# Performance work log

Measured on AMD Instinct MI355X. Metric: run time of the kernel, lower is better.

Reference implementation:

```python
import jax, jax.numpy as jnp
import numpy as np
import math

M = 8                      # multiplicity (channels per irrep)
COMBOS = [(0,0,0),(0,1,1),(1,0,1),(1,1,0),(1,1,1),(2,1,1)]  # (edge_l, node_l, out_l)

def _cg_coeff(j1, m1, j2, m2, j3, m3):
    # standard (Racah) complex Clebsch-Gordan coefficient <j1 m1 j2 m2 | j3 m3>
    if m3 != m1 + m2:
        return 0.0
    f = math.factorial
    vmin = max(0, j2 - j3 - m1, j1 + m2 - j3)
    vmax = min(j1 + j2 - j3, j1 - m1, j2 + m2)
    pref = (2*j3 + 1) * f(j3+j1-j2) * f(j3-j1+j2) * f(j1+j2-j3) / f(j1+j2+j3+1)
    pref *= f(j3+m3) * f(j3-m3) * f(j1-m1) * f(j1+m1) * f(j2-m2) * f(j2+m2)
    s = 0.0
    for v in range(vmin, vmax + 1):
        s += (-1)**v / (f(v) * f(j1+j2-j3-v) * f(j1-m1-v) * f(j2+m2-v)
                        * f(j3-j2+m1+v) * f(j3-j1-m2+v))
    return math.sqrt(pref) * s

def _su2_cg(l1, l2, l3):
    C = np.zeros((2*l1+1, 2*l2+1, 2*l3+1), dtype=np.complex128)
    for m1 in range(-l1, l1+1):
        for m2 in range(-l2, l2+1):
            m3 = m1 + m2
            if -l3 <= m3 <= l3:
                C[m1+l1, m2+l2, m3+l3] = _cg_coeff(l1, m1, l2, m2, l3, m3)
    return C

def _qmat(l):
    # real -> complex spherical-harmonic change of basis (e3nn convention)
    q = np.zeros((2*l+1, 2*l+1), dtype=np.complex128)
    for m in range(-l, 0):
        q[l+m, l+abs(m)] = 1/np.sqrt(2)
        q[l+m, l-abs(m)] = -1j/np.sqrt(2)
    q[l, l] = 1.0
    for m in range(1, l+1):
        q[l+m, l+abs(m)] = (-1)**m / np.sqrt(2)
        q[l+m, l-abs(m)] = 1j * (-1)**m / np.sqrt(2)
    return (-1j)**l * q

def _so3_cg(l1, l2, l3):
    # real-basis CG, normalized to unit Frobenius norm (matches e3nn _so3_clebsch_gordan)
    C = np.einsum('ij,kl,mn,ikn->jlm', _qmat(l1), _qmat(l2),
                  np.conj(_qmat(l3)).T, _su2_cg(l1, l2, l3))
    assert np.abs(C.imag).max() < 1e-6
    C = C.real
    return C / np.linalg.norm(C)

CG = {c: jnp.asarray(_so3_cg(*c), dtype=jnp.float32) for c in COMBOS}


def setup_inputs() -> dict:
    N, E = 100000, 1600000
    ks = jax.random.split(jax.random.key(0), 6)
    return {
        'node_irreps': jax.random.normal(ks[0], (N, 4*M), jnp.float32),
        'edge_index': jax.random.randint(ks[1], (2, E), 0, N, dtype=jnp.int32),
        'sh0': jax.random.normal(ks[2], (E, 1), jnp.float32),
        'sh1': jax.random.normal(ks[3], (E, 3), jnp.float32),
        'sh2': jax.random.normal(ks[4], (E, 5), jnp.float32),
        'W': jax.random.normal(ks[5], (len(COMBOS), M, M), jnp.float32),
    }


def reference(node_irreps, edge_index, sh0, sh1, sh2, W):
    N, E = node_irreps.shape[0], edge_index.shape[1]
    src = node_irreps[edge_index[0]]                    # gather: [E, 4M]
    feats = {0: src[:, :M][:, :, None],                 # scalar channels [E, M, 1]
             1: src[:, M:].reshape(E, M, 3)}            # vector channels [E, M, 3]
    sh = {0: sh0, 1: sh1, 2: sh2}
    msg = {0: jnp.zeros((E, M, 1), node_irreps.dtype),
           1: jnp.zeros((E, M, 3), node_irreps.dtype)}
    for idx, (le, ln, lo) in enumerate(COMBOS):
        # per-edge CG tensor product: [de,dn,do] x [E,de] x [E,M,dn] -> [E,M,do]
        base = jnp.einsum('ijk,ei,emj->emk', CG[(le, ln, lo)], sh[le], feats[ln])
        # channel-mixing scalar weights (in_channel -> out_channel)
        msg[lo] = msg[lo] + jnp.einsum('io,eik->eok', W[idx], base)
    tgt = edge_index[1]
    agg0 = jax.ops.segment_sum(msg[0].reshape(E, M), tgt, num_segments=N)     # [N, M]
    agg1 = jax.ops.segment_sum(msg[1].reshape(E, 3*M), tgt, num_segments=N)   # [N, 3M]
    return jnp.concatenate([agg0, agg1], axis=1)
```

## Files before the change

kernel.cpp:

```cpp
#include <hip/hip_runtime.h>

#define THREADS 256

typedef float v4f __attribute__((ext_vector_type(4)));


__global__ __launch_bounds__(THREADS) void k_hist2(const int* __restrict__ tgt,
                                                   int* __restrict__ cnt,
                                                   int* __restrict__ ke, int E) {
    int e = blockIdx.x * THREADS + threadIdx.x;
    if (e < E) ke[e] = atomicAdd(&cnt[tgt[e]], 1);
}

__global__ __launch_bounds__(THREADS) void k_scan_partial(const int* __restrict__ cnt,
                                                          int* __restrict__ bsum, int N) {
    __shared__ int lds[THREADS];
    int base = blockIdx.x * 1024 + threadIdx.x * 4;
    int s = 0;
    #pragma unroll
    for (int k = 0; k < 4; ++k) { int i = base + k; if (i < N) s += cnt[i]; }
    lds[threadIdx.x] = s; __syncthreads();
    for (int off = THREADS / 2; off > 0; off >>= 1) {
        if (threadIdx.x < off) lds[threadIdx.x] += lds[threadIdx.x + off];
        __syncthreads();
    }
    if (threadIdx.x == 0) bsum[blockIdx.x] = lds[0];
}

__global__ __launch_bounds__(1024) void k_scan_bsum(int* __restrict__ bsum, int NB) {
    __shared__ int lds[1024];
    int t = threadIdx.x;
    int v = (t < NB) ? bsum[t] : 0;
    lds[t] = v; __syncthreads();
    for (int off = 1; off < 1024; off <<= 1) {
        int x = (t >= off) ? lds[t - off] : 0;
        __syncthreads();
        lds[t] += x;
        __syncthreads();
    }
    if (t < NB) bsum[t] = lds[t] - v;
}

__global__ __launch_bounds__(THREADS) void k_scan_final(const int* __restrict__ cnt,
                                                        const int* __restrict__ bsum,
                                                        int* __restrict__ rowptr,
                                                        int N, int E) {
    __shared__ int lds[THREADS];
    int base = blockIdx.x * 1024 + threadIdx.x * 4;
    int v[4]; int local = 0;
    #pragma unroll
    for (int k = 0; k < 4; ++k) {
        int i = base + k;
        v[k] = (i < N) ? cnt[i] : 0;
        local += v[k];
    }
    lds[threadIdx.x] = local; __syncthreads();
    for (int off = 1; off < THREADS; off <<= 1) {
        int x = (threadIdx.x >= off) ? lds[threadIdx.x - off] : 0;
        __syncthreads();
        lds[threadIdx.x] += x;
        __syncthreads();
    }
    int p = lds[threadIdx.x] - local + bsum[blockIdx.x];
    #pragma unroll
    for (int k = 0; k < 4; ++k) {
        int i = base + k;
        if (i < N) { rowptr[i] = p; p += v[k]; }
    }
    if (blockIdx.x == 0 && threadIdx.x == 0) rowptr[N] = E;
}


__global__ __launch_bounds__(THREADS) void k_scatter(const int* __restrict__ eidx,
                                                     const int* __restrict__ ke,
                                                     const int* __restrict__ rowptr,
                                                     const float* __restrict__ sh0,
                                                     const float* __restrict__ sh1,
                                                     const float* __restrict__ sh2,
                                                     float* __restrict__ payload,
                                                     int E) {
    int e = blockIdx.x * THREADS + threadIdx.x;
    if (e >= E) return;
    int src = eidx[e];
    int tgt = eidx[E + e];
    int pos = rowptr[tgt] + ke[e];

    float4 p0 = make_float4(sh0[e], sh1[3*e+0], sh1[3*e+1], sh1[3*e+2]);
    float4 p1 = make_float4(sh2[5*e+0], sh2[5*e+1], sh2[5*e+2], sh2[5*e+3]);
    float4 p2 = make_float4(sh2[5*e+4], __int_as_float(src), 0.f, 0.f);
    float4 p3 = make_float4(0.f, 0.f, 0.f, 0.f);

    float4* pr = (float4*)(payload + (size_t)pos * 16);
    pr[0] = p0; pr[1] = p1; pr[2] = p2; pr[3] = p3;
}


#define ACC_STRIDE 15

__global__ __launch_bounds__(THREADS) void k_agg2(const float* __restrict__ node,
                                                  const int*   __restrict__ rowptr,
                                                  const float* __restrict__ payload,
                                                  const float* __restrict__ W,
                                                  float*       __restrict__ out, int N) {
    __shared__ float sW[384];
    __shared__ float sAcc[32 * 8 * ACC_STRIDE];
    for (int t = threadIdx.x; t < 384; t += THREADS) sW[t] = W[t];
    __syncthreads();

    constexpr float IS3  = 0.57735026918962576f;
    constexpr float IS6  = 0.40824829046386302f;
    constexpr float IS10 = 0.31622776601683794f;
    constexpr float IS30 = 0.18257418583505536f;

    const int nodeSlot = threadIdx.x >> 3;
    const int i        = threadIdx.x & 7;
    const int n        = blockIdx.x * 32 + nodeSlot;

    float a[14];
    #pragma unroll
    for (int k = 0; k < 14; ++k) a[k] = 0.f;

    if (n < N) {
        const int jbeg = rowptr[n];
        const int jend = rowptr[n + 1];

        if (jbeg < jend) {
            const v4f* pr = (const v4f*)(payload + (size_t)jbeg * 16);
            v4f c0 = __builtin_nontemporal_load(pr + 0);
            v4f c1 = __builtin_nontemporal_load(pr + 1);
            v4f c2 = __builtin_nontemporal_load(pr + 2);

            for (int j = jbeg; j < jend; ++j) {
                v4f n0, n1, n2;
                if (j + 1 < jend) {
                    const v4f* prn = (const v4f*)(payload + (size_t)(j + 1) * 16);
                    n0 = __builtin_nontemporal_load(prn + 0);
                    n1 = __builtin_nontemporal_load(prn + 1);
                    n2 = __builtin_nontemporal_load(prn + 2);
                }

                const int src = __float_as_int(c2.y);
                const float* nr = node + (size_t)src * 32;
                const float f0 = nr[i];
                const float x  = nr[8 + 3*i + 0];
                const float y  = nr[8 + 3*i + 1];
                const float z  = nr[8 + 3*i + 2];

                const float s  = c0.x, u0 = c0.y, u1 = c0.z, u2 = c0.w;
                const float q0 = c1.x, q1 = c1.y, q2 = c1.z, q3 = c1.w, q4 = c2.x;

                const float Q00 = -q2*IS30 - q4*IS10;
                const float Q01 =  q1*IS10;
                const float Q02 =  q0*IS10;
                const float Q11 =  2.0f*q2*IS30;
                const float Q12 =  q3*IS10;
                const float Q22 = -q2*IS30 + q4*IS10;

                a[0]  += s * f0;
                a[1]  += u0*x + u1*y + u2*z;
                a[2]  += s * x;
                a[3]  += s * y;
                a[4]  += s * z;
                a[5]  += f0 * u0;
                a[6]  += f0 * u1;
                a[7]  += f0 * u2;
                a[8]  += u1*z - u2*y;
                a[9]  += u2*x - u0*z;
                a[10] += u0*y - u1*x;
                a[11] += Q00*x + Q01*y + Q02*z;
                a[12] += Q01*x + Q11*y + Q12*z;
                a[13] += Q02*x + Q12*y + Q22*z;

                c0 = n0; c1 = n1; c2 = n2;
            }
        }
    }

    #pragma unroll
    for (int k = 1; k < 8; ++k) a[k] *= IS3;
    #pragma unroll
    for (int k = 8; k < 11; ++k) a[k] *= IS6;

    float* myAcc = &sAcc[(nodeSlot * 8 + i) * ACC_STRIDE];
    #pragma unroll
    for (int k = 0; k < 14; ++k) myAcc[k] = a[k];
    __syncthreads();

    if (n < N) {
        const int o = i;
        float o0 = 0.f, ox = 0.f, oy = 0.f, oz = 0.f;
        #pragma unroll
        for (int ii = 0; ii < 8; ++ii) {
            const float* A = &sAcc[(nodeSlot * 8 + ii) * ACC_STRIDE];
            const float w0 = sW[  0 + ii*8 + o];
            const float w1 = sW[ 64 + ii*8 + o];
            const float w2 = sW[128 + ii*8 + o];
            const float w3 = sW[192 + ii*8 + o];
            const float w4 = sW[256 + ii*8 + o];
            const float w5 = sW[320 + ii*8 + o];
            o0 += w0*A[0]  + w3*A[1];
            ox += w1*A[2]  + w2*A[5] + w4*A[8]  + w5*A[11];
            oy += w1*A[3]  + w2*A[6] + w4*A[9]  + w5*A[12];
            oz += w1*A[4]  + w2*A[7] + w4*A[10] + w5*A[13];
        }
        float* orow = out + (size_t)n * 32;
        orow[o]         = o0;
        orow[8 + 3*o+0] = ox;
        orow[8 + 3*o+1] = oy;
        orow[8 + 3*o+2] = oz;
    }
}


__global__ __launch_bounds__(THREADS) void msg_kernel_atomic(
    const float* __restrict__ node,
    const int*   __restrict__ eidx,
    const float* __restrict__ sh0,
    const float* __restrict__ sh1,
    const float* __restrict__ sh2,
    const float* __restrict__ W,
    float*       __restrict__ out,
    int E)
{
    __shared__ float sW[384];
    for (int t = threadIdx.x; t < 384; t += THREADS) sW[t] = W[t];
    __syncthreads();

    int e = blockIdx.x * THREADS + threadIdx.x;
    if (e >= E) return;

    constexpr float IS3  = 0.57735026918962576f;
    constexpr float IS6  = 0.40824829046386302f;
    constexpr float IS10 = 0.31622776601683794f;
    constexpr float IS30 = 0.18257418583505536f;

    const int src = eidx[e];
    const int tgt = eidx[E + e];

    const float s  = sh0[e];
    const float u0 = sh1[3*e+0], u1 = sh1[3*e+1], u2 = sh1[3*e+2];
    const float q0 = sh2[5*e+0], q1 = sh2[5*e+1], q2 = sh2[5*e+2],
                q3 = sh2[5*e+3], q4 = sh2[5*e+4];

    const float Q00 = -q2*IS30 - q4*IS10;
    const float Q01 =  q1*IS10;
    const float Q02 =  q0*IS10;
    const float Q11 =  2.0f*q2*IS30;
    const float Q12 =  q3*IS10;
    const float Q22 = -q2*IS30 + q4*IS10;

    float f[32];
    {
        const float4* nr = (const float4*)(node + (size_t)src * 32);
        #pragma unroll
        for (int i = 0; i < 8; ++i) {
            float4 v = nr[i];
            f[4*i+0]=v.x; f[4*i+1]=v.y; f[4*i+2]=v.z; f[4*i+3]=v.w;
        }
    }

    float msg[32];
    #pragma unroll
    for (int j = 0; j < 32; ++j) msg[j] = 0.0f;

    const float s13 = s * IS3;

    #pragma unroll
    for (int i = 0; i < 8; ++i) {
        const float f0i = f[i];
        const float x = f[8+3*i+0], y = f[8+3*i+1], z = f[8+3*i+2];
        const float c0  = s * f0i;
        const float c3  = IS3 * (u0*x + u1*y + u2*z);
        const float p2  = IS3 * f0i;
        const float c1x = s13*x, c1y = s13*y, c1z = s13*z;
        const float c2x = p2*u0, c2y = p2*u1, c2z = p2*u2;
        const float c4x = IS6*(u1*z - u2*y);
        const float c4y = IS6*(u2*x - u0*z);
        const float c4z = IS6*(u0*y - u1*x);
        const float c5x = Q00*x + Q01*y + Q02*z;
        const float c5y = Q01*x + Q11*y + Q12*z;
        const float c5z = Q02*x + Q12*y + Q22*z;

        float wr[6][8];
        #pragma unroll
        for (int c = 0; c < 6; ++c) {
            float4 aa = *(const float4*)&sW[c*64 + i*8 + 0];
            float4 bb = *(const float4*)&sW[c*64 + i*8 + 4];
            wr[c][0]=aa.x; wr[c][1]=aa.y; wr[c][2]=aa.z; wr[c][3]=aa.w;
            wr[c][4]=bb.x; wr[c][5]=bb.y; wr[c][6]=bb.z; wr[c][7]=bb.w;
        }

        #pragma unroll
        for (int o = 0; o < 8; ++o) {
            msg[o] += wr[0][o]*c0 + wr[3][o]*c3;
            msg[8+3*o+0] += wr[1][o]*c1x + wr[2][o]*c2x + wr[4][o]*c4x + wr[5][o]*c5x;
            msg[8+3*o+1] += wr[1][o]*c1y + wr[2][o]*c2y + wr[4][o]*c4y + wr[5][o]*c5y;
            msg[8+3*o+2] += wr[1][o]*c1z + wr[2][o]*c2z + wr[4][o]*c4z + wr[5][o]*c5z;
        }
    }

    float* orow = out + (size_t)tgt * 32;
    #pragma unroll
    for (int j = 0; j < 32; ++j) unsafeAtomicAdd(orow + j, msg[j]);
}


extern "C" void kernel_launch(void* const* d_in, const int* in_sizes, int n_in,
                              void* d_out, int out_size, void* d_ws, size_t ws_size,
                              hipStream_t stream) {
    const float* node = (const float*)d_in[0];
    const int*   eidx = (const int*)d_in[1];
    const float* sh0  = (const float*)d_in[2];
    const float* sh1  = (const float*)d_in[3];
    const float* sh2  = (const float*)d_in[4];
    const float* W    = (const float*)d_in[5];
    float* out = (float*)d_out;

    const int E = in_sizes[2];
    const int N = in_sizes[0] / 32;
    const int NB = (N + 1023) / 1024;

    size_t int_words = (size_t)(N + 1) + N + 1024 + (size_t)E;
    size_t pay_off_w = (int_words + 15) & ~(size_t)15;
    size_t need      = (pay_off_w + (size_t)E * 16) * sizeof(float);

    if (ws_size >= need && NB <= 1024) {
        int* rowptr = (int*)d_ws;
        int* cnt    = rowptr + (N + 1);
        int* bsum   = cnt + N;
        int* ke     = bsum + 1024;
        float* payload = (float*)d_ws + pay_off_w;

        hipMemsetAsync(cnt, 0, (size_t)N * sizeof(int), stream);

        k_hist2<<<(E + THREADS - 1) / THREADS, THREADS, 0, stream>>>(eidx + E, cnt, ke, E);
        k_scan_partial<<<NB, THREADS, 0, stream>>>(cnt, bsum, N);
        k_scan_bsum<<<1, 1024, 0, stream>>>(bsum, NB);
        k_scan_final<<<NB, THREADS, 0, stream>>>(cnt, bsum, rowptr, N, E);
        k_scatter<<<(E + THREADS - 1) / THREADS, THREADS, 0, stream>>>(
            eidx, ke, rowptr, sh0, sh1, sh2, payload, E);

        k_agg2<<<(N + 31) / 32, THREADS, 0, stream>>>(node, rowptr, payload, W, out, N);
    } else {
        hipMemsetAsync(d_out, 0, (size_t)out_size * sizeof(float), stream);
        msg_kernel_atomic<<<(E + THREADS - 1) / THREADS, THREADS, 0, stream>>>(
            node, eidx, sh0, sh1, sh2, W, out, E);
    }
}
```

Baseline: 346.6 us.

## Replace per-edge payload scatter with compact edge-index CSR and transposed node layout

Instead of scattering a 64-byte payload per edge (sh values plus src) into CSR order, the scatter now writes only an (edge id, src) pair using an atomic cursor, and the aggregation kernel gathers sh0/sh1/sh2 directly by edge id. Node features are pre-transposed so each lane loads its scalar and vector channel with one 16-byte load, and the per-edge ke array is dropped. This cuts scatter write traffic and workspace, but adds random gathers of sh arrays in the aggregation loop and a second atomic pass.

```diff
diff --git a/kernel.cpp b/kernel.cpp
--- a/kernel.cpp
+++ b/kernel.cpp
@@ -3,13 +3,13 @@
 #define THREADS 256
 
 typedef float v4f __attribute__((ext_vector_type(4)));
-
-
-__global__ __launch_bounds__(THREADS) void k_hist2(const int* __restrict__ tgt,
-                                                   int* __restrict__ cnt,
-                                                   int* __restrict__ ke, int E) {
+typedef int   v2i __attribute__((ext_vector_type(2)));
+
+
+__global__ __launch_bounds__(THREADS) void k_hist(const int* __restrict__ tgt,
+                                                  int* __restrict__ cnt, int E) {
     int e = blockIdx.x * THREADS + threadIdx.x;
-    if (e < E) ke[e] = atomicAdd(&cnt[tgt[e]], 1);
+    if (e < E) atomicAdd(&cnt[tgt[e]], 1);
 }
 
 __global__ __launch_bounds__(THREADS) void k_scan_partial(const int* __restrict__ cnt,
@@ -41,7 +41,7 @@
     if (t < NB) bsum[t] = lds[t] - v;
 }
 
-__global__ __launch_bounds__(THREADS) void k_scan_final(const int* __restrict__ cnt,
+__global__ __launch_bounds__(THREADS) void k_scan_final(int* __restrict__ cnt,
                                                         const int* __restrict__ bsum,
                                                         int* __restrict__ rowptr,
                                                         int N, int E) {
@@ -65,41 +65,48 @@
     #pragma unroll
     for (int k = 0; k < 4; ++k) {
         int i = base + k;
-        if (i < N) { rowptr[i] = p; p += v[k]; }
+        if (i < N) { rowptr[i] = p; cnt[i] = p; p += v[k]; }
     }
     if (blockIdx.x == 0 && threadIdx.x == 0) rowptr[N] = E;
 }
 
 
-__global__ __launch_bounds__(THREADS) void k_scatter(const int* __restrict__ eidx,
-                                                     const int* __restrict__ ke,
-                                                     const int* __restrict__ rowptr,
-                                                     const float* __restrict__ sh0,
-                                                     const float* __restrict__ sh1,
-                                                     const float* __restrict__ sh2,
-                                                     float* __restrict__ payload,
-                                                     int E) {
+__global__ __launch_bounds__(THREADS) void k_ntrans(const float* __restrict__ node,
+                                                    float* __restrict__ nodeT, int NT8) {
+    int t = blockIdx.x * THREADS + threadIdx.x;
+    if (t >= NT8) return;
+    int n = t >> 3, i = t & 7;
+    const float* nr = node + (size_t)n * 32;
+    v4f v;
+    v[0] = nr[i];
+    v[1] = nr[8 + 3*i + 0];
+    v[2] = nr[8 + 3*i + 1];
+    v[3] = nr[8 + 3*i + 2];
+    *(v4f*)(nodeT + (size_t)t * 4) = v;
+}
+
+
+__global__ __launch_bounds__(THREADS) void k_scatter2(const int* __restrict__ eidx,
+                                                      int* __restrict__ cursor,
+                                                      int* __restrict__ col2, int E) {
     int e = blockIdx.x * THREADS + threadIdx.x;
     if (e >= E) return;
     int src = eidx[e];
     int tgt = eidx[E + e];
-    int pos = rowptr[tgt] + ke[e];
-
-    float4 p0 = make_float4(sh0[e], sh1[3*e+0], sh1[3*e+1], sh1[3*e+2]);
-    float4 p1 = make_float4(sh2[5*e+0], sh2[5*e+1], sh2[5*e+2], sh2[5*e+3]);
-    float4 p2 = make_float4(sh2[5*e+4], __int_as_float(src), 0.f, 0.f);
-    float4 p3 = make_float4(0.f, 0.f, 0.f, 0.f);
-
-    float4* pr = (float4*)(payload + (size_t)pos * 16);
-    pr[0] = p0; pr[1] = p1; pr[2] = p2; pr[3] = p3;
+    int pos = atomicAdd(&cursor[tgt], 1);
+    v2i v; v[0] = e; v[1] = src;
+    *(v2i*)(col2 + 2*(size_t)pos) = v;
 }
 
 
 #define ACC_STRIDE 15
 
-__global__ __launch_bounds__(THREADS) void k_agg2(const float* __restrict__ node,
+__global__ __launch_bounds__(THREADS) void k_agg3(const float* __restrict__ nodeT,
                                                   const int*   __restrict__ rowptr,
-                                                  const float* __restrict__ payload,
+                                                  const int*   __restrict__ col2,
+                                                  const float* __restrict__ sh0,
+                                                  const float* __restrict__ sh1,
+                                                  const float* __restrict__ sh2,
                                                   const float* __restrict__ W,
                                                   float*       __restrict__ out, int N) {
     __shared__ float sW[384];
@@ -125,29 +132,35 @@
         const int jend = rowptr[n + 1];
 
         if (jbeg < jend) {
-            const v4f* pr = (const v4f*)(payload + (size_t)jbeg * 16);
-            v4f c0 = __builtin_nontemporal_load(pr + 0);
-            v4f c1 = __builtin_nontemporal_load(pr + 1);
-            v4f c2 = __builtin_nontemporal_load(pr + 2);
+            const int jlast = jend - 1;
+
+            v2i ec = __builtin_nontemporal_load((const v2i*)(col2 + 2*(size_t)jbeg));
+            {
+            }
+            const int e0 = ec[0];
+            float s  = sh0[e0];
+            const float* up = sh1 + 3*(size_t)e0;
+            float u0 = up[0], u1 = up[1], u2 = up[2];
+            const float* qp = sh2 + 5*(size_t)e0;
+            float q0 = qp[0], q1 = qp[1], q2 = qp[2], q3 = qp[3], q4 = qp[4];
+            v4f nf = *(const v4f*)(nodeT + ((size_t)ec[1] * 8 + i) * 4);
+
+            int jn1 = (jbeg + 1 < jend) ? jbeg + 1 : jlast;
+            v2i ecn = __builtin_nontemporal_load((const v2i*)(col2 + 2*(size_t)jn1));
 
             for (int j = jbeg; j < jend; ++j) {
-                v4f n0, n1, n2;
-                if (j + 1 < jend) {
-                    const v4f* prn = (const v4f*)(payload + (size_t)(j + 1) * 16);
-                    n0 = __builtin_nontemporal_load(prn + 0);
-                    n1 = __builtin_nontemporal_load(prn + 1);
-                    n2 = __builtin_nontemporal_load(prn + 2);
-                }
-
-                const int src = __float_as_int(c2.y);
-                const float* nr = node + (size_t)src * 32;
-                const float f0 = nr[i];
-                const float x  = nr[8 + 3*i + 0];
-                const float y  = nr[8 + 3*i + 1];
-                const float z  = nr[8 + 3*i + 2];
-
-                const float s  = c0.x, u0 = c0.y, u1 = c0.z, u2 = c0.w;
-                const float q0 = c1.x, q1 = c1.y, q2 = c1.z, q3 = c1.w, q4 = c2.x;
+                const int en = ecn[0];
+                const float ns = sh0[en];
+                const float* nup = sh1 + 3*(size_t)en;
+                const float nu0 = nup[0], nu1 = nup[1], nu2 = nup[2];
+                const float* nqp = sh2 + 5*(size_t)en;
+                const float nq0 = nqp[0], nq1 = nqp[1], nq2 = nqp[2],
+                            nq3 = nqp[3], nq4 = nqp[4];
+                const v4f nnf = *(const v4f*)(nodeT + ((size_t)ecn[1] * 8 + i) * 4);
+                const int jn2 = (j + 2 < jend) ? j + 2 : jlast;
+                const v2i ec2 = __builtin_nontemporal_load((const v2i*)(col2 + 2*(size_t)jn2));
+
+                const float f0 = nf[0], x = nf[1], y = nf[2], z = nf[3];
 
                 const float Q00 = -q2*IS30 - q4*IS10;
                 const float Q01 =  q1*IS10;
@@ -171,7 +184,9 @@
                 a[12] += Q01*x + Q11*y + Q12*z;
                 a[13] += Q02*x + Q12*y + Q22*z;
 
-                c0 = n0; c1 = n1; c2 = n2;
+                s = ns; u0 = nu0; u1 = nu1; u2 = nu2;
+                q0 = nq0; q1 = nq1; q2 = nq2; q3 = nq3; q4 = nq4;
+                nf = nnf; ecn = ec2;
             }
         }
     }
@@ -320,27 +335,35 @@
     const int N = in_sizes[0] / 32;
     const int NB = (N + 1023) / 1024;
 
-    size_t int_words = (size_t)(N + 1) + N + 1024 + (size_t)E;
-    size_t pay_off_w = (int_words + 15) & ~(size_t)15;
-    size_t need      = (pay_off_w + (size_t)E * 16) * sizeof(float);
+    size_t off = 0;
+    size_t off_rowptr = off; off += (size_t)N + 1;
+    size_t off_cnt    = off; off += (size_t)N;
+    size_t off_bsum   = off; off += 1024;
+    off = (off + 3) & ~(size_t)3;
+    size_t off_col2   = off; off += 2 * (size_t)E;
+    off = (off + 3) & ~(size_t)3;
+    size_t off_nodeT  = off; off += 32 * (size_t)N;
+    size_t need = off * sizeof(float);
 
     if (ws_size >= need && NB <= 1024) {
-        int* rowptr = (int*)d_ws;
-        int* cnt    = rowptr + (N + 1);
-        int* bsum   = cnt + N;
-        int* ke     = bsum + 1024;
-        float* payload = (float*)d_ws + pay_off_w;
+        int* wsI    = (int*)d_ws;
+        int* rowptr = wsI + off_rowptr;
+        int* cnt    = wsI + off_cnt;
+        int* bsum   = wsI + off_bsum;
+        int* col2   = wsI + off_col2;
+        float* nodeT = (float*)d_ws + off_nodeT;
 
         hipMemsetAsync(cnt, 0, (size_t)N * sizeof(int), stream);
 
-        k_hist2<<<(E + THREADS - 1) / THREADS, THREADS, 0, stream>>>(eidx + E, cnt, ke, E);
+        k_hist<<<(E + THREADS - 1) / THREADS, THREADS, 0, stream>>>(eidx + E, cnt, E);
+        k_ntrans<<<(8 * N + THREADS - 1) / THREADS, THREADS, 0, stream>>>(node, nodeT, 8 * N);
         k_scan_partial<<<NB, THREADS, 0, stream>>>(cnt, bsum, N);
         k_scan_bsum<<<1, 1024, 0, stream>>>(bsum, NB);
         k_scan_final<<<NB, THREADS, 0, stream>>>(cnt, bsum, rowptr, N, E);
-        k_scatter<<<(E + THREADS - 1) / THREADS, THREADS, 0, stream>>>(
-            eidx, ke, rowptr, sh0, sh1, sh2, payload, E);
-
-        k_agg2<<<(N + 31) / 32, THREADS, 0, stream>>>(node, rowptr, payload, W, out, N);
+        k_scatter2<<<(E + THREADS - 1) / THREADS, THREADS, 0, stream>>>(eidx, cnt, col2, E);
+
+        k_agg3<<<(N + 31) / 32, THREADS, 0, stream>>>(nodeT, rowptr, col2,
+                                                      sh0, sh1, sh2, W, out, N);
     } else {
         hipMemsetAsync(d_out, 0, (size_t)out_size * sizeof(float), stream);
         msg_kernel_atomic<<<(E + THREADS - 1) / THREADS, THREADS, 0, stream>>>(
```

Result: slower. 468.4 us (+35.1%).

## Write edge payload in edge order with CSR index indirection and deeper prefetch

Applied to the files above, without the earlier changes.

The pack kernel now writes the per-edge spherical-harmonic payload in original edge order with the quadrupole matrix precomputed, so those writes are coalesced rather than scattered. Only a small CSR column array of edge ids is scattered. The aggregation kernel then reads the payload and source ids indirectly through that array and prefetches node features one edge ahead. A fallback path uses an atomic cursor when the workspace is too small to hold the per-edge rank array. The cost is that aggregation reads become random 64-byte gathers plus an extra dependent load chain (col, then esrc, then node).

```diff
diff --git a/kernel.cpp b/kernel.cpp
--- a/kernel.cpp
+++ b/kernel.cpp
@@ -10,6 +10,12 @@
                                                    int* __restrict__ ke, int E) {
     int e = blockIdx.x * THREADS + threadIdx.x;
     if (e < E) ke[e] = atomicAdd(&cnt[tgt[e]], 1);
+}
+
+__global__ __launch_bounds__(THREADS) void k_hist(const int* __restrict__ tgt,
+                                                  int* __restrict__ cnt, int E) {
+    int e = blockIdx.x * THREADS + threadIdx.x;
+    if (e < E) atomicAdd(&cnt[tgt[e]], 1);
 }
 
 __global__ __launch_bounds__(THREADS) void k_scan_partial(const int* __restrict__ cnt,
@@ -41,7 +47,7 @@
     if (t < NB) bsum[t] = lds[t] - v;
 }
 
-__global__ __launch_bounds__(THREADS) void k_scan_final(const int* __restrict__ cnt,
+__global__ __launch_bounds__(THREADS) void k_scan_final(int* __restrict__ cnt,
                                                         const int* __restrict__ bsum,
                                                         int* __restrict__ rowptr,
                                                         int N, int E) {
@@ -65,41 +71,66 @@
     #pragma unroll
     for (int k = 0; k < 4; ++k) {
         int i = base + k;
-        if (i < N) { rowptr[i] = p; p += v[k]; }
+        if (i < N) { rowptr[i] = p; cnt[i] = p; p += v[k]; }
     }
     if (blockIdx.x == 0 && threadIdx.x == 0) rowptr[N] = E;
 }
 
 
-__global__ __launch_bounds__(THREADS) void k_scatter(const int* __restrict__ eidx,
-                                                     const int* __restrict__ ke,
-                                                     const int* __restrict__ rowptr,
-                                                     const float* __restrict__ sh0,
-                                                     const float* __restrict__ sh1,
-                                                     const float* __restrict__ sh2,
-                                                     float* __restrict__ payload,
-                                                     int E) {
+__global__ __launch_bounds__(THREADS) void k_pack(const int* __restrict__ eidx,
+                                                  const int* __restrict__ ke,
+                                                  const int* __restrict__ rowptr,
+                                                  int* __restrict__ cursor,
+                                                  int* __restrict__ col,
+                                                  const float* __restrict__ sh0,
+                                                  const float* __restrict__ sh1,
+                                                  const float* __restrict__ sh2,
+                                                  float* __restrict__ pack,
+                                                  int E) {
     int e = blockIdx.x * THREADS + threadIdx.x;
     if (e >= E) return;
-    int src = eidx[e];
-    int tgt = eidx[E + e];
-    int pos = rowptr[tgt] + ke[e];
-
-    float4 p0 = make_float4(sh0[e], sh1[3*e+0], sh1[3*e+1], sh1[3*e+2]);
-    float4 p1 = make_float4(sh2[5*e+0], sh2[5*e+1], sh2[5*e+2], sh2[5*e+3]);
-    float4 p2 = make_float4(sh2[5*e+4], __int_as_float(src), 0.f, 0.f);
-    float4 p3 = make_float4(0.f, 0.f, 0.f, 0.f);
-
-    float4* pr = (float4*)(payload + (size_t)pos * 16);
-    pr[0] = p0; pr[1] = p1; pr[2] = p2; pr[3] = p3;
+
+    constexpr float IS10 = 0.31622776601683794f;
+    constexpr float IS30 = 0.18257418583505536f;
+
+    const int tgt = eidx[E + e];
+    int pos;
+    if (ke) pos = rowptr[tgt] + ke[e];
+    else    pos = atomicAdd(&cursor[tgt], 1);
+    col[pos] = e;
+
+    const float s  = __builtin_nontemporal_load(&sh0[e]);
+    const float u0 = __builtin_nontemporal_load(&sh1[3*e+0]);
+    const float u1 = __builtin_nontemporal_load(&sh1[3*e+1]);
+    const float u2 = __builtin_nontemporal_load(&sh1[3*e+2]);
+    const float q0 = __builtin_nontemporal_load(&sh2[5*e+0]);
+    const float q1 = __builtin_nontemporal_load(&sh2[5*e+1]);
+    const float q2 = __builtin_nontemporal_load(&sh2[5*e+2]);
+    const float q3 = __builtin_nontemporal_load(&sh2[5*e+3]);
+    const float q4 = __builtin_nontemporal_load(&sh2[5*e+4]);
+
+    const float Q00 = -q2*IS30 - q4*IS10;
+    const float Q01 =  q1*IS10;
+    const float Q02 =  q0*IS10;
+    const float Q11 =  2.0f*q2*IS30;
+    const float Q12 =  q3*IS10;
+    const float Q22 = -q2*IS30 + q4*IS10;
+
+    float4* pr = (float4*)(pack + (size_t)e * 16);
+    pr[0] = make_float4(s, u0, u1, u2);
+    pr[1] = make_float4(Q00, Q01, Q02, Q11);
+    pr[2] = make_float4(Q12, Q22, 0.f, 0.f);
+    pr[3] = make_float4(0.f, 0.f, 0.f, 0.f);
 }
 
 
 #define ACC_STRIDE 15
 
-__global__ __launch_bounds__(THREADS) void k_agg2(const float* __restrict__ node,
+__global__ __launch_bounds__(THREADS) void k_agg5(const float* __restrict__ node,
                                                   const int*   __restrict__ rowptr,
-                                                  const float* __restrict__ payload,
+                                                  const int*   __restrict__ col,
+                                                  const int*   __restrict__ esrc,
+                                                  const float* __restrict__ pack,
                                                   const float* __restrict__ W,
                                                   float*       __restrict__ out, int N) {
     __shared__ float sW[384];
@@ -109,8 +140,6 @@
 
     constexpr float IS3  = 0.57735026918962576f;
     constexpr float IS6  = 0.40824829046386302f;
-    constexpr float IS10 = 0.31622776601683794f;
-    constexpr float IS30 = 0.18257418583505536f;
 
     const int nodeSlot = threadIdx.x >> 3;
     const int i        = threadIdx.x & 7;
@@ -125,36 +154,41 @@
         const int jend = rowptr[n + 1];
 
         if (jbeg < jend) {
-            const v4f* pr = (const v4f*)(payload + (size_t)jbeg * 16);
-            v4f c0 = __builtin_nontemporal_load(pr + 0);
-            v4f c1 = __builtin_nontemporal_load(pr + 1);
-            v4f c2 = __builtin_nontemporal_load(pr + 2);
+            const int jlast = jend - 1;
+
+            const int e0 = __builtin_nontemporal_load(&col[jbeg]);
+            const int s0 = esrc[e0];
+            const v4f* pp = (const v4f*)(pack + (size_t)e0 * 16);
+            v4f c0 = __builtin_nontemporal_load(pp + 0);
+            v4f c1 = __builtin_nontemporal_load(pp + 1);
+            v4f c2 = __builtin_nontemporal_load(pp + 2);
+            const float* nr0 = node + (size_t)s0 * 32;
+            float f0 = nr0[i];
+            float x  = nr0[8 + 3*i + 0];
+            float y  = nr0[8 + 3*i + 1];
+            float z  = nr0[8 + 3*i + 2];
+
+            const int j1 = (jbeg + 1 < jend) ? jbeg + 1 : jlast;
+            int eA = __builtin_nontemporal_load(&col[j1]);
+            int sA = esrc[eA];
 
             for (int j = jbeg; j < jend; ++j) {
-                v4f n0, n1, n2;
-                if (j + 1 < jend) {
-                    const v4f* prn = (const v4f*)(payload + (size_t)(j + 1) * 16);
-                    n0 = __builtin_nontemporal_load(prn + 0);
-                    n1 = __builtin_nontemporal_load(prn + 1);
-                    n2 = __builtin_nontemporal_load(prn + 2);
-                }
-
-                const int src = __float_as_int(c2.y);
-                const float* nr = node + (size_t)src * 32;
-                const float f0 = nr[i];
-                const float x  = nr[8 + 3*i + 0];
-                const float y  = nr[8 + 3*i + 1];
-                const float z  = nr[8 + 3*i + 2];
-
-                const float s  = c0.x, u0 = c0.y, u1 = c0.z, u2 = c0.w;
-                const float q0 = c1.x, q1 = c1.y, q2 = c1.z, q3 = c1.w, q4 = c2.x;
-
-                const float Q00 = -q2*IS30 - q4*IS10;
-                const float Q01 =  q1*IS10;
-                const float Q02 =  q0*IS10;
-                const float Q11 =  2.0f*q2*IS30;
-                const float Q12 =  q3*IS10;
-                const float Q22 = -q2*IS30 + q4*IS10;
+                const v4f* pn = (const v4f*)(pack + (size_t)eA * 16);
+                const v4f n0 = __builtin_nontemporal_load(pn + 0);
+                const v4f n1 = __builtin_nontemporal_load(pn + 1);
+                const v4f n2 = __builtin_nontemporal_load(pn + 2);
+                const float* nrn = node + (size_t)sA * 32;
+                const float nf0 = nrn[i];
+                const float nx  = nrn[8 + 3*i + 0];
+                const float ny  = nrn[8 + 3*i + 1];
+                const float nz  = nrn[8 + 3*i + 2];
+                const int j2 = (j + 2 < jend) ? j + 2 : jlast;
+                const int eB = __builtin_nontemporal_load(&col[j2]);
+                const int sB = esrc[eB];
+
+                const float s  = c0[0], u0 = c0[1], u1 = c0[2], u2 = c0[3];
+                const float Q00 = c1[0], Q01 = c1[1], Q02 = c1[2], Q11 = c1[3];
+                const float Q12 = c2[0], Q22 = c2[1];
 
                 a[0]  += s * f0;
                 a[1]  += u0*x + u1*y + u2*z;
@@ -172,6 +206,8 @@
                 a[13] += Q02*x + Q12*y + Q22*z;
 
                 c0 = n0; c1 = n1; c2 = n2;
+                f0 = nf0; x = nx; y = ny; z = nz;
+                eA = eB; sA = sB;
             }
         }
     }
@@ -320,30 +356,46 @@
     const int N = in_sizes[0] / 32;
     const int NB = (N + 1023) / 1024;
 
-    size_t int_words = (size_t)(N + 1) + N + 1024 + (size_t)E;
-    size_t pay_off_w = (int_words + 15) & ~(size_t)15;
-    size_t need      = (pay_off_w + (size_t)E * 16) * sizeof(float);
-
-    if (ws_size >= need && NB <= 1024) {
-        int* rowptr = (int*)d_ws;
+    size_t base_w = (size_t)(N + 1) + N + 1024;
+    size_t intA_w = base_w + (size_t)E + (size_t)E;
+    size_t intB_w = base_w + (size_t)E;
+    size_t packA_off = (intA_w + 15) & ~(size_t)15;
+    size_t packB_off = (intB_w + 15) & ~(size_t)15;
+    size_t needA = (packA_off + (size_t)E * 16) * sizeof(float);
+    size_t needB = (packB_off + (size_t)E * 16) * sizeof(float);
+
+    const int gridE = (E + THREADS - 1) / THREADS;
+
+    if (ws_size >= needB && NB <= 1024) {
+        const bool useKe = (ws_size >= needA);
+
+        int* wsI    = (int*)d_ws;
+        int* rowptr = wsI;
         int* cnt    = rowptr + (N + 1);
         int* bsum   = cnt + N;
-        int* ke     = bsum + 1024;
-        float* payload = (float*)d_ws + pay_off_w;
+        int* ke     = useKe ? (bsum + 1024) : nullptr;
+        int* col    = useKe ? (ke + E) : (bsum + 1024);
+        float* pack = (float*)d_ws + (useKe ? packA_off : packB_off);
 
         hipMemsetAsync(cnt, 0, (size_t)N * sizeof(int), stream);
 
-        k_hist2<<<(E + THREADS - 1) / THREADS, THREADS, 0, stream>>>(eidx + E, cnt, ke, E);
+        if (useKe)
+            k_hist2<<<gridE, THREADS, 0, stream>>>(eidx + E, cnt, ke, E);
+        else
+            k_hist<<<gridE, THREADS, 0, stream>>>(eidx + E, cnt, E);
+
         k_scan_partial<<<NB, THREADS, 0, stream>>>(cnt, bsum, N);
         k_scan_bsum<<<1, 1024, 0, stream>>>(bsum, NB);
         k_scan_final<<<NB, THREADS, 0, stream>>>(cnt, bsum, rowptr, N, E);
-        k_scatter<<<(E + THREADS - 1) / THREADS, THREADS, 0, stream>>>(
-            eidx, ke, rowptr, sh0, sh1, sh2, payload, E);
-
-        k_agg2<<<(N + 31) / 32, THREADS, 0, stream>>>(node, rowptr, payload, W, out, N);
+
+        k_pack<<<gridE, THREADS, 0, stream>>>(eidx, ke, rowptr, cnt, col,
+                                              sh0, sh1, sh2, pack, E);
+
+        k_agg5<<<(N + 31) / 32, THREADS, 0, stream>>>(node, rowptr, col, eidx,
+                                                      pack, W, out, N);
     } else {
         hipMemsetAsync(d_out, 0, (size_t)out_size * sizeof(float), stream);
-        msg_kernel_atomic<<<(E + THREADS - 1) / THREADS, THREADS, 0, stream>>>(
+        msg_kernel_atomic<<<gridE, THREADS, 0, stream>>>(
             node, eidx, sh0, sh1, sh2, W, out, E);
     }
 }
```

Result: slower. 424.2 us (+22.4%).
